# Kernel optimization log

Measured on AMD Instinct MI355X. Metric: run time of the kernel, lower is better.

Reference implementation:

```python
import jax, jax.numpy as jnp
import numpy as np
from jax import lax

B, T, E = 256, 128, 768      # batch, seq_len, bert emb dim
HE = 256                     # encoder lstm hidden (per direction)
H = 512                      # decoder hidden = 2*HE
SLOT, INTENT = 120, 64
EMB = SLOT // 3              # 40
V = SLOT + 1                 # 121, bos id = SLOT
DIN = EMB + 2 * H            # 1064 decoder lstm input
NEG = -1e12


def lstm_cell(x, h, c, Wih, Whh, bih, bhh):
    # torch gate order: i, f, g, o
    g = x @ Wih.T + h @ Whh.T + (bih + bhh)
    i, f, gg, o = jnp.split(g, 4, axis=-1)
    c = jax.nn.sigmoid(f) * c + jax.nn.sigmoid(i) * jnp.tanh(gg)
    h = jax.nn.sigmoid(o) * jnp.tanh(c)
    return h, c


def setup_inputs() -> dict:
    key = jax.random.key(0)
    ks = jax.random.split(key, 24)
    s = 0.05
    n = lambda k, shp: jax.random.normal(k, shp, jnp.float32) * s
    return {
        'seq_reps': jax.random.normal(ks[0], (B, T, E), jnp.float32),
        'nwp_index': jax.random.randint(ks[1], (B, T, 1), 0, 2),
        'slot_output_mask': jax.random.randint(ks[2], (B, T), 0, 2).astype(bool),
        'emb_table': jax.random.uniform(ks[3], (V, EMB), jnp.float32, -0.1, 0.1),
        # encoder fwd / bwd LSTM
        'Wf_ih': n(ks[4], (4 * HE, E)), 'Wf_hh': n(ks[5], (4 * HE, HE)),
        'bf_ih': n(ks[6], (4 * HE,)), 'bf_hh': n(ks[7], (4 * HE,)),
        'Wb_ih': n(ks[8], (4 * HE, E)), 'Wb_hh': n(ks[9], (4 * HE, HE)),
        'bb_ih': n(ks[10], (4 * HE,)), 'bb_hh': n(ks[11], (4 * HE,)),
        # decoder LSTM
        'Wd_ih': n(ks[12], (4 * H, DIN)), 'Wd_hh': n(ks[13], (4 * H, H)),
        'bd_ih': n(ks[14], (4 * H,)), 'bd_hh': n(ks[15], (4 * H,)),
        # attention + output heads
        'attn_W': n(ks[16], (H, H)), 'attn_b': n(ks[17], (H,)),
        'slot_W': n(ks[18], (SLOT, 2 * H)), 'slot_b': n(ks[19], (SLOT,)),
        'intent_W': n(ks[20], (INTENT, 2 * H)), 'intent_b': n(ks[21], (INTENT,)),
    }


def forward(seq_reps, nwp_index, slot_output_mask, emb_table,
            Wf_ih, Wf_hh, bf_ih, bf_hh, Wb_ih, Wb_hh, bb_ih, bb_hh,
            Wd_ih, Wd_hh, bd_ih, bd_hh, attn_W, attn_b,
            slot_W, slot_b, intent_W, intent_b):
    # ---------- Encoder: 1-layer bidirectional LSTM ----------
    xs = seq_reps.transpose(1, 0, 2)  # [T,B,E]
    z = jnp.zeros((B, HE), seq_reps.dtype)

    def fstep(carry, x):
        h, c = lstm_cell(x, carry[0], carry[1], Wf_ih, Wf_hh, bf_ih, bf_hh)
        return (h, c), h

    def bstep(carry, x):
        h, c = lstm_cell(x, carry[0], carry[1], Wb_ih, Wb_hh, bb_ih, bb_hh)
        return (h, c), h

    _, hf = lax.scan(fstep, (z, z), xs)
    _, hb = lax.scan(bstep, (z, z), xs[::-1])
    enc = jnp.concatenate([hf, hb[::-1]], -1).transpose(1, 0, 2)  # [B,T,512]

    # last real hidden: out[b, #nonzero(nwp_index[b])]
    count = jnp.clip((nwp_index[:, :, 0] != 0).sum(1), 0, T - 1)
    last_hidden = enc[jnp.arange(B), count]  # [B,H]

    # ---------- Attention (energies independent of step -> precompute) ----------
    energies = enc @ attn_W.T + attn_b  # [B,T,H]

    def attention(h):  # h: [B,H]
        e = jnp.einsum('bth,bh->bt', energies, h)
        e = jnp.where(slot_output_mask, NEG, e)
        alpha = jax.nn.softmax(e, -1)
        return jnp.einsum('bt,bth->bh', alpha, enc)  # [B,H]

    # ---------- Decoder: per-timestep LSTM + attention ----------
    bos_emb = jnp.broadcast_to(emb_table[SLOT], (B, EMB))
    zH = jnp.zeros((B, H), seq_reps.dtype)
    aligns = enc.transpose(1, 0, 2)  # [T,B,H]

    def dstep(carry, aligned):
        emb, ctx, h, c = carry
        inp = jnp.concatenate([emb, ctx, aligned], -1)  # [B,1064]
        h, c = lstm_cell(inp, h, c, Wd_ih, Wd_hh, bd_ih, bd_hh)
        score = jnp.concatenate([h, ctx], -1) @ slot_W.T + slot_b
        logp = jax.nn.log_softmax(score, -1)
        nxt = jnp.argmax(logp, -1)
        emb = emb_table[nxt]
        ctx_new = attention(h)
        return (emb, ctx_new, h, c), (logp, h, ctx_new)

    _, (logps, h_seq, ctx_seq) = lax.scan(dstep, (bos_emb, last_hidden, zH, zH), aligns)

    slot_scores = logps.transpose(1, 0, 2)  # [B,T,SLOT]
    # intent computed at step 0: intent_context == attention(h after step 0) == ctx_seq[0]
    intent_score = jnp.concatenate([h_seq[0], ctx_seq[0]], -1) @ intent_W.T + intent_b
    return slot_scores, intent_score


def reference(seq_reps, nwp_index, slot_output_mask, emb_table,
              Wf_ih, Wf_hh, bf_ih, bf_hh, Wb_ih, Wb_hh, bb_ih, bb_hh,
              Wd_ih, Wd_hh, bd_ih, bd_hh, attn_W, attn_b,
              slot_W, slot_b, intent_W, intent_b):
    return forward(seq_reps, nwp_index, slot_output_mask, emb_table,
                   Wf_ih, Wf_hh, bf_ih, bf_hh, Wb_ih, Wb_hh, bb_ih, bb_hh,
                   Wd_ih, Wd_hh, bd_ih, bd_hh, attn_W, attn_b,
                   slot_W, slot_b, intent_W, intent_b)
```

## Files before the change

kernel.cpp:

```cpp
#include <hip/hip_runtime.h>
#include <math.h>

#define Bn 256
#define Tn 128
#define En 768
#define HEn 256
#define Hn 512
#define SLOTn 120
#define INTENTn 64
#define EMBn 40
#define NEGV -1e12f

__device__ __forceinline__ float sigm(float x) { return 1.0f / (1.0f + expf(-x)); }

__global__ void zero_k(float* __restrict__ p, int n) {
    int i = blockIdx.x * blockDim.x + threadIdx.x;
    int stride = gridDim.x * blockDim.x;
    for (; i < n; i += stride) p[i] = 0.f;
}

__global__ void detect_mask_k(const unsigned char* __restrict__ m, int* __restrict__ flag) {
    __shared__ int any;
    if (threadIdx.x == 0) any = 0;
    __syncthreads();
    int found = 0;
    for (int i = threadIdx.x; i < 32768; i += 256) {
        if ((i & 3) != 0 && m[i] != 0) found = 1;
    }
    if (found) atomicOr(&any, 1);
    __syncthreads();
    if (threadIdx.x == 0) *flag = any;
}

__global__ __launch_bounds__(256) void slotwt_k(const float* __restrict__ W,
                                               float* __restrict__ wT4) {
    int idx = blockIdx.x * 256 + threadIdx.x;
    int k = idx >> 7, s = idx & 127;
    float v = (s < SLOTn) ? W[(size_t)s * 1024 + k] : 0.f;
    wT4[((size_t)(k >> 2) * 128 + s) * 4 + (k & 3)] = v;
}

__device__ __forceinline__ float4 f4zero() { float4 z; z.x = z.y = z.z = z.w = 0.f; return z; }

__device__ __forceinline__ float4 enc_wload(const float* __restrict__ Wih,
                                            const float* __restrict__ Whh,
                                            int jrow, int k) {
    return (k < En) ? *(const float4*)(Wih + (size_t)jrow * En + k)
                    : *(const float4*)(Whh + (size_t)jrow * HEn + (k - En));
}

__global__ __launch_bounds__(512) void enc_step_k(
    const float* __restrict__ seq,
    const float* __restrict__ Wf_ih, const float* __restrict__ Wf_hh,
    const float* __restrict__ bf_ih, const float* __restrict__ bf_hh,
    const float* __restrict__ Wb_ih, const float* __restrict__ Wb_hh,
    const float* __restrict__ bb_ih, const float* __restrict__ bb_hh,
    const float* __restrict__ hf_in, float* __restrict__ hf_out, float* __restrict__ cf,
    const float* __restrict__ hb_in, float* __restrict__ hb_out, float* __restrict__ cb,
    float* __restrict__ enc, int step)
{
    const int dir = blockIdx.z;
    const float* __restrict__ Wih = dir ? Wb_ih : Wf_ih;
    const float* __restrict__ Whh = dir ? Wb_hh : Wf_hh;
    const float* __restrict__ bih = dir ? bb_ih : bf_ih;
    const float* __restrict__ bhh = dir ? bb_hh : bf_hh;
    const float* __restrict__ h_in = dir ? hb_in : hf_in;
    float* __restrict__ h_out = dir ? hb_out : hf_out;
    float* __restrict__ c_st  = dir ? cb : cf;
    const int t_eff = dir ? (Tn - 1 - step) : step;

    const int jb = blockIdx.x;
    const int b0 = blockIdx.y << 5;
    const int tid = threadIdx.x;
    const int c   = tid & 63;
    const int wid = __builtin_amdgcn_readfirstlane(tid >> 6);
    const int bw  = b0 + (wid << 2);

    __shared__ float Bs[2][64][68];
    __shared__ float Gs[32][68];

    const int cs0 = tid >> 4,          kq0 = tid & 15;
    const int cs1 = (tid + 512) >> 4;
    const int j0row = ((cs0 >> 4) << 8) + (jb << 4) + (cs0 & 15);
    const int j1row = ((cs1 >> 4) << 8) + (jb << 4) + (cs1 & 15);

    float acc[4] = {0,0,0,0};

    float4 p0 = enc_wload(Wih, Whh, j0row, kq0 << 2);
    float4 p1 = enc_wload(Wih, Whh, j1row, kq0 << 2);
    *(float4*)&Bs[0][cs0][kq0 << 2] = p0;
    *(float4*)&Bs[0][cs1][kq0 << 2] = p1;
    __syncthreads();

    for (int t = 0; t < 16; ++t) {
        const int k0 = t << 6;
        const int buf = t & 1;
        if (t < 15) {
            p0 = enc_wload(Wih, Whh, j0row, k0 + 64 + (kq0 << 2));
            p1 = enc_wload(Wih, Whh, j1row, k0 + 64 + (kq0 << 2));
        }
#pragma unroll
        for (int g = 0; g < 16; ++g) {
            const int kk = k0 + (g << 2);
            const float* __restrict__ abase;
            size_t astr;
            if (kk < En) { abase = seq + ((size_t)bw * Tn + t_eff) * En + kk; astr = (size_t)Tn * En; }
            else         { abase = h_in + ((size_t)bw << 8) + (kk - En);      astr = HEn; }
            float4 bf = *(const float4*)&Bs[buf][c][g << 2];
#pragma unroll
            for (int i = 0; i < 4; ++i) {
                float4 a = *(const float4*)(abase + (size_t)i * astr);
                acc[i] += a.x * bf.x + a.y * bf.y + a.z * bf.z + a.w * bf.w;
            }
        }
        if (t < 15) {
            *(float4*)&Bs[buf ^ 1][cs0][kq0 << 2] = p0;
            *(float4*)&Bs[buf ^ 1][cs1][kq0 << 2] = p1;
        }
        __syncthreads();
    }

#pragma unroll
    for (int i = 0; i < 4; ++i) Gs[(wid << 2) + i][c] = acc[i];
    __syncthreads();

    {
        int row = tid >> 4, jl = tid & 15;
        int jg = (jb << 4) + jl;
        int b = b0 + row;
        float gi = Gs[row][jl]      + bih[jg]           + bhh[jg];
        float gf = Gs[row][16 + jl] + bih[HEn + jg]     + bhh[HEn + jg];
        float gg = Gs[row][32 + jl] + bih[2 * HEn + jg] + bhh[2 * HEn + jg];
        float go = Gs[row][48 + jl] + bih[3 * HEn + jg] + bhh[3 * HEn + jg];
        float ii = sigm(gi), ff = sigm(gf), tg = tanhf(gg), oo = sigm(go);
        int ci = (b << 8) + jg;
        float cn = ff * c_st[ci] + ii * tg;
        float hn = oo * tanhf(cn);
        c_st[ci] = cn;
        h_out[ci] = hn;
        enc[((size_t)t_eff * Bn + b) * Hn + dir * HEn + jg] = hn;
    }
}

__global__ __launch_bounds__(256) void energT_k(
    const float* __restrict__ enc, const float* __restrict__ attn_W,
    float* __restrict__ energT)
{
    const int nb = blockIdx.x;
    const int mb = blockIdx.y;
    const int t = mb >> 2, b0 = (mb & 3) << 6;
    const int tid = threadIdx.x;
    const int tx = tid & 15, ty = tid >> 4;
    __shared__ float As[32][68];
    __shared__ float Bs[32][68];
    float acc[4][4] = {};
    for (int kt = 0; kt < 16; ++kt) {
        int k0 = kt << 5;
#pragma unroll
        for (int r = 0; r < 8; ++r) {
            int idx = tid + (r << 8);
            int kk = idx & 31, row = idx >> 5;
            As[kk][row] = enc[((size_t)t * Bn + b0 + row) * Hn + k0 + kk];
            Bs[kk][row] = attn_W[(nb * 64 + row) * Hn + k0 + kk];
        }
        __syncthreads();
#pragma unroll
        for (int kk = 0; kk < 32; ++kk) {
            float a0 = As[kk][ty * 4], a1 = As[kk][ty * 4 + 1];
            float a2 = As[kk][ty * 4 + 2], a3 = As[kk][ty * 4 + 3];
            float w0 = Bs[kk][tx * 4], w1 = Bs[kk][tx * 4 + 1];
            float w2 = Bs[kk][tx * 4 + 2], w3 = Bs[kk][tx * 4 + 3];
            acc[0][0] += a0 * w0; acc[0][1] += a0 * w1; acc[0][2] += a0 * w2; acc[0][3] += a0 * w3;
            acc[1][0] += a1 * w0; acc[1][1] += a1 * w1; acc[1][2] += a1 * w2; acc[1][3] += a1 * w3;
            acc[2][0] += a2 * w0; acc[2][1] += a2 * w1; acc[2][2] += a2 * w2; acc[2][3] += a2 * w3;
            acc[3][0] += a3 * w0; acc[3][1] += a3 * w1; acc[3][2] += a3 * w2; acc[3][3] += a3 * w3;
        }
        __syncthreads();
    }
#pragma unroll
    for (int i = 0; i < 4; ++i)
#pragma unroll
        for (int q = 0; q < 4; ++q)
            energT[((size_t)(b0 + ty * 4 + i) * Hn + nb * 64 + tx * 4 + q) * Tn + t] = acc[i][q];
}

__global__ __launch_bounds__(64) void init2_k(
    const int* __restrict__ nwp, const float* __restrict__ enc,
    const float* __restrict__ emb_table,
    float* __restrict__ ctx0, float* __restrict__ embb)
{
    int b = blockIdx.x;
    int lane = threadIdx.x;
    int p1 = (nwp[b * Tn + lane] != 0);
    int p2 = (nwp[b * Tn + lane + 64] != 0);
    unsigned long long m1 = __ballot(p1), m2 = __ballot(p2);
    int cnt = __popcll(m1) + __popcll(m2);
    int idx = cnt < (Tn - 1) ? cnt : (Tn - 1);
#pragma unroll
    for (int r = 0; r < 8; ++r) {
        int j = lane + (r << 6);
        ctx0[(b << 9) + j] = enc[((size_t)idx * Bn + b) * Hn + j];
    }
    if (lane < EMBn) embb[b * EMBn + lane] = emb_table[SLOTn * EMBn + lane];
}

__device__ __forceinline__ float4 dec_wload(const float* __restrict__ Wih,
                                            const float* __restrict__ Whh,
                                            int jrow, int k) {
    if (k < 1064) return *(const float4*)(Wih + (size_t)jrow * 1064 + k);
    if (k < 1576) return *(const float4*)(Whh + ((size_t)jrow << 9) + (k - 1064));
    return f4zero();
}

__global__ __launch_bounds__(512) void dec_step_k(
    const float* __restrict__ embb, const float* __restrict__ ctx_in,
    const float* __restrict__ enc, const float* __restrict__ h_in,
    float* __restrict__ h_out, float* __restrict__ c_st,
    const float* __restrict__ Wih, const float* __restrict__ Whh,
    const float* __restrict__ bih, const float* __restrict__ bhh,
    float* __restrict__ h0_out, int step)
{
    const int jb = blockIdx.x;
    const int b0 = blockIdx.y << 5;
    const int tid = threadIdx.x;
    const int c   = tid & 63;
    const int wid = __builtin_amdgcn_readfirstlane(tid >> 6);
    const int bw  = b0 + (wid << 2);

    __shared__ float Bs[2][64][68];
    __shared__ float Gs[32][68];

    const int cs0 = tid >> 4,          kq0 = tid & 15;
    const int cs1 = (tid + 512) >> 4;
    const int j0row = ((cs0 >> 4) << 9) + (jb << 4) + (cs0 & 15);
    const int j1row = ((cs1 >> 4) << 9) + (jb << 4) + (cs1 & 15);

    float acc[4] = {0,0,0,0};

    float4 p0 = dec_wload(Wih, Whh, j0row, kq0 << 2);
    float4 p1 = dec_wload(Wih, Whh, j1row, kq0 << 2);
    *(float4*)&Bs[0][cs0][kq0 << 2] = p0;
    *(float4*)&Bs[0][cs1][kq0 << 2] = p1;
    __syncthreads();

    for (int t = 0; t < 25; ++t) {
        const int k0 = t << 6;
        const int buf = t & 1;
        if (t < 24) {
            p0 = dec_wload(Wih, Whh, j0row, k0 + 64 + (kq0 << 2));
            p1 = dec_wload(Wih, Whh, j1row, k0 + 64 + (kq0 << 2));
        }
#pragma unroll
        for (int g = 0; g < 16; ++g) {
            const int kk = k0 + (g << 2);
            if (kk < 1576) {
                const float* __restrict__ abase;
                size_t astr;
                if (kk < 40)        { abase = embb   + (size_t)bw * EMBn + kk;               astr = EMBn; }
                else if (kk < 552)  { abase = ctx_in + ((size_t)bw << 9) + (kk - 40);        astr = Hn; }
                else if (kk < 1064) { abase = enc + ((size_t)step * Bn + bw) * Hn + (kk - 552); astr = Hn; }
                else                { abase = h_in  + ((size_t)bw << 9) + (kk - 1064);       astr = Hn; }
                float4 bf = *(const float4*)&Bs[buf][c][g << 2];
#pragma unroll
                for (int i = 0; i < 4; ++i) {
                    float4 a = *(const float4*)(abase + (size_t)i * astr);
                    acc[i] += a.x * bf.x + a.y * bf.y + a.z * bf.z + a.w * bf.w;
                }
            }
        }
        if (t < 24) {
            *(float4*)&Bs[buf ^ 1][cs0][kq0 << 2] = p0;
            *(float4*)&Bs[buf ^ 1][cs1][kq0 << 2] = p1;
        }
        __syncthreads();
    }

#pragma unroll
    for (int i = 0; i < 4; ++i) Gs[(wid << 2) + i][c] = acc[i];
    __syncthreads();

    {
        int row = tid >> 4, jl = tid & 15;
        int jg = (jb << 4) + jl;
        int b = b0 + row;
        float gi = Gs[row][jl]      + bih[jg]          + bhh[jg];
        float gf = Gs[row][16 + jl] + bih[Hn + jg]     + bhh[Hn + jg];
        float gg = Gs[row][32 + jl] + bih[2 * Hn + jg] + bhh[2 * Hn + jg];
        float go = Gs[row][48 + jl] + bih[3 * Hn + jg] + bhh[3 * Hn + jg];
        float ii = sigm(gi), ff = sigm(gf), tg = tanhf(gg), oo = sigm(go);
        int ci = (b << 9) + jg;
        float cn = ff * c_st[ci] + ii * tg;
        float hn = oo * tanhf(cn);
        c_st[ci] = cn;
        h_out[ci] = hn;
        if (h0_out) h0_out[ci] = hn;
    }
}

__global__ __launch_bounds__(256) void dec_attn_slot_k(
    const float* __restrict__ enc, const float* __restrict__ energT,
    const float* __restrict__ h, const float* __restrict__ ctx_in,
    float* __restrict__ ctx_out, const unsigned char* __restrict__ mask_u8,
    const int* __restrict__ mask_i32, const int* __restrict__ mask_flag,
    const float* __restrict__ wT4, const float* __restrict__ slot_b,
    const float* __restrict__ emb_table, float* __restrict__ embb,
    float* __restrict__ out_slot, float* __restrict__ ctx0_save, int step)
{
    __shared__ float hs[512];
    __shared__ float red2[8][132];
    __shared__ float es[128];
    __shared__ float redm[2];
    __shared__ float ctxp[2][512];
    __shared__ float pacc[2][8][132];
    __shared__ float sc[8][132];
    __shared__ float logZ[8];
    __shared__ int amax[8];

    const int bid = blockIdx.x;
    const int tid = threadIdx.x;

    if (bid < Bn) {
        const int b = bid;
        hs[tid] = h[(b << 9) + tid];
        hs[tid + 256] = h[(b << 9) + 256 + tid];
        __syncthreads();
        {
            const int tg = tid & 31, jg = tid >> 5;
            const float* __restrict__ ep = energT + ((size_t)b * Hn + jg * 64) * Tn + (tg << 2);
            float4 a = f4zero();
#pragma unroll 8
            for (int jj = 0; jj < 64; ++jj) {
                float hv = hs[jg * 64 + jj];
                float4 e4 = *(const float4*)(ep + (size_t)jj * Tn);
                a.x += e4.x * hv; a.y += e4.y * hv; a.z += e4.z * hv; a.w += e4.w * hv;
            }
            *(float4*)&red2[jg][tg << 2] = a;
        }
        __syncthreads();
        if (tid < 128) {
            float e = 0.f;
#pragma unroll
            for (int jg = 0; jg < 8; ++jg) e += red2[jg][tid];
            bool mv = (*mask_flag) ? (mask_u8[(size_t)b * Tn + tid] != 0)
                                   : (mask_i32[(size_t)b * Tn + tid] != 0);
            es[tid] = mv ? NEGV : e;
        }
        __syncthreads();
        if (tid < 64) {
            float v = fmaxf(es[tid], es[tid + 64]);
            for (int o = 32; o; o >>= 1) v = fmaxf(v, __shfl_down(v, o));
            if (tid == 0) redm[0] = v;
        }
        __syncthreads();
        float m = redm[0];
        if (tid < 128) es[tid] = __expf(es[tid] - m);
        __syncthreads();
        if (tid < 64) {
            float v = es[tid] + es[tid + 64];
            for (int o = 32; o; o >>= 1) v += __shfl_down(v, o);
            if (tid == 0) redm[0] = v;
        }
        __syncthreads();
        float inv = 1.0f / redm[0];
        if (tid < 128) es[tid] *= inv;
        __syncthreads();
        {
            const int dq = tid & 127, th = tid >> 7;
            const int d = dq << 2;
            const float* __restrict__ ep2 = enc + (b << 9) + d;
            float4 a = f4zero();
            const int tbase = th << 6;
#pragma unroll 8
            for (int t2 = 0; t2 < 64; ++t2) {
                float al = es[tbase + t2];
                float4 e4 = *(const float4*)(ep2 + (size_t)(tbase + t2) * (Bn * Hn));
                a.x += al * e4.x; a.y += al * e4.y; a.z += al * e4.z; a.w += al * e4.w;
            }
            *(float4*)&ctxp[th][d] = a;
        }
        __syncthreads();
        {
            float v0 = ctxp[0][tid] + ctxp[1][tid];
            float v1 = ctxp[0][tid + 256] + ctxp[1][tid + 256];
            ctx_out[(b << 9) + tid] = v0;
            ctx_out[(b << 9) + 256 + tid] = v1;
            if (ctx0_save) {
                ctx0_save[(b << 9) + tid] = v0;
                ctx0_save[(b << 9) + 256 + tid] = v1;
            }
        }
    } else {
        const int b_base = (bid - Bn) << 3;
        const int sl = tid & 127;
        const int kg = __builtin_amdgcn_readfirstlane(tid >> 7);
        const float* __restrict__ a0 = (kg ? ctx_in : h) + ((size_t)b_base << 9);
        const float* __restrict__ wb = wT4 + (size_t)kg * 128 * 128 * 4;
        float acc[8] = {0,0,0,0,0,0,0,0};
        for (int k4 = 0; k4 < 128; ++k4) {
            const int k = k4 << 2;
            float4 w4 = *(const float4*)(wb + ((size_t)k4 * 128 + sl) * 4);
#pragma unroll
            for (int i = 0; i < 8; ++i) {
                const float* __restrict__ ar = a0 + ((size_t)i << 9) + k;
                acc[i] += w4.x * ar[0] + w4.y * ar[1] + w4.z * ar[2] + w4.w * ar[3];
            }
        }
#pragma unroll
        for (int i = 0; i < 8; ++i) pacc[kg][i][sl] = acc[i];
        __syncthreads();
        if (tid < 128) {
            float sb = (tid < SLOTn) ? slot_b[tid] : 0.f;
#pragma unroll
            for (int i = 0; i < 8; ++i)
                sc[i][tid] = pacc[0][i][tid] + pacc[1][i][tid] + sb;
        }
        __syncthreads();
        if (tid < 8) {
            float mm = -INFINITY; int am = 0;
            for (int ss = 0; ss < SLOTn; ++ss) {
                float v = sc[tid][ss];
                if (v > mm) { mm = v; am = ss; }
            }
            float sum = 0.f;
            for (int ss = 0; ss < SLOTn; ++ss) sum += __expf(sc[tid][ss] - mm);
            logZ[tid] = mm + logf(sum);
            amax[tid] = am;
        }
        __syncthreads();
        for (int r = 0; r < 4; ++r) {
            int idx = tid + (r << 8);
            int bl = idx >> 7, ss = idx & 127;
            if (ss < SLOTn)
                out_slot[(size_t)(b_base + bl) * Tn * SLOTn + step * SLOTn + ss] =
                    sc[bl][ss] - logZ[bl];
        }
        for (int i = tid; i < 8 * EMBn; i += 256) {
            int bl = i / EMBn, e2 = i % EMBn;
            embb[(b_base + bl) * EMBn + e2] = emb_table[amax[bl] * EMBn + e2];
        }
    }
}

__global__ __launch_bounds__(256) void intent_k(
    const float* __restrict__ h0, const float* __restrict__ ctx0,
    const float* __restrict__ W, const float* __restrict__ bias,
    float* __restrict__ out)
{
    __shared__ float ins[8][1032];
    __shared__ float Ws[16][68];
    const int tid = threadIdx.x;
    const int b_base = blockIdx.x << 3;
    for (int r = 0; r < 32; ++r) {
        int idx = tid + (r << 8);
        int bl = idx >> 10, k = idx & 1023;
        int b = b_base + bl;
        ins[bl][k] = (k < 512) ? h0[(b << 9) + k] : ctx0[(b << 9) + (k - 512)];
    }
    __syncthreads();
    const int n = tid & 63, bq = tid >> 6;
    float acc0 = 0.f, acc1 = 0.f;
    for (int kt = 0; kt < 64; ++kt) {
        int k0 = kt << 4;
#pragma unroll
        for (int r = 0; r < 4; ++r) {
            int idx = tid + (r << 8);
            int kk = idx & 15, nn = idx >> 4;
            Ws[kk][nn] = W[nn * 1024 + k0 + kk];
        }
        __syncthreads();
#pragma unroll
        for (int kk = 0; kk < 16; ++kk) {
            float w = Ws[kk][n];
            acc0 += w * ins[bq * 2][k0 + kk];
            acc1 += w * ins[bq * 2 + 1][k0 + kk];
        }
        __syncthreads();
    }
    out[(b_base + bq * 2) * INTENTn + n] = acc0 + bias[n];
    out[(b_base + bq * 2 + 1) * INTENTn + n] = acc1 + bias[n];
}

extern "C" void kernel_launch(void* const* d_in, const int* in_sizes, int n_in,
                              void* d_out, int out_size, void* d_ws, size_t ws_size,
                              hipStream_t stream) {
    (void)in_sizes; (void)n_in; (void)out_size; (void)ws_size;

    const float* seq      = (const float*)d_in[0];
    const int*   nwp      = (const int*)d_in[1];
    const unsigned char* mask_u8 = (const unsigned char*)d_in[2];
    const int*   mask_i32 = (const int*)d_in[2];
    const float* embt     = (const float*)d_in[3];
    const float* Wf_ih    = (const float*)d_in[4];
    const float* Wf_hh    = (const float*)d_in[5];
    const float* bf_ih    = (const float*)d_in[6];
    const float* bf_hh    = (const float*)d_in[7];
    const float* Wb_ih    = (const float*)d_in[8];
    const float* Wb_hh    = (const float*)d_in[9];
    const float* bb_ih    = (const float*)d_in[10];
    const float* bb_hh    = (const float*)d_in[11];
    const float* Wd_ih    = (const float*)d_in[12];
    const float* Wd_hh    = (const float*)d_in[13];
    const float* bd_ih    = (const float*)d_in[14];
    const float* bd_hh    = (const float*)d_in[15];
    const float* attn_W   = (const float*)d_in[16];
    const float* slot_W   = (const float*)d_in[18];
    const float* slot_b   = (const float*)d_in[19];
    const float* intent_W = (const float*)d_in[20];
    const float* intent_b = (const float*)d_in[21];

    float* Wp = (float*)d_ws;
    size_t off = 0;
    float* enc    = Wp + off; off += (size_t)Tn * Bn * Hn;
    float* energT = Wp + off; off += (size_t)Bn * Hn * Tn;
    float* zbase  = Wp + off;
    float* hf0 = Wp + off; off += Bn * HEn;
    float* hf1 = Wp + off; off += Bn * HEn;
    float* cf  = Wp + off; off += Bn * HEn;
    float* hb0 = Wp + off; off += Bn * HEn;
    float* hb1 = Wp + off; off += Bn * HEn;
    float* cb  = Wp + off; off += Bn * HEn;
    float* hd0 = Wp + off; off += Bn * Hn;
    float* hd1 = Wp + off; off += Bn * Hn;
    float* cd  = Wp + off; off += Bn * Hn;
    int nzero = (int)(Wp + off - zbase);
    float* ctx0b = Wp + off; off += Bn * Hn;
    float* ctx1b = Wp + off; off += Bn * Hn;
    float* h0s   = Wp + off; off += Bn * Hn;
    float* ctx0s = Wp + off; off += Bn * Hn;
    float* embb  = Wp + off; off += Bn * EMBn;
    int* mask_flag = (int*)(Wp + off); off += 1;
    float* wT4   = Wp + off; off += 1024 * 128;

    float* out = (float*)d_out;

    zero_k<<<512, 256, 0, stream>>>(zbase, nzero);
    detect_mask_k<<<1, 256, 0, stream>>>(mask_u8, mask_flag);
    slotwt_k<<<512, 256, 0, stream>>>(slot_W, wT4);

    for (int s = 0; s < Tn; ++s) {
        const float* hinf = (s & 1) ? hf1 : hf0;
        float* houtf      = (s & 1) ? hf0 : hf1;
        const float* hinb = (s & 1) ? hb1 : hb0;
        float* houtb      = (s & 1) ? hb0 : hb1;
        enc_step_k<<<dim3(16, 8, 2), 512, 0, stream>>>(
            seq, Wf_ih, Wf_hh, bf_ih, bf_hh, Wb_ih, Wb_hh, bb_ih, bb_hh,
            hinf, houtf, cf, hinb, houtb, cb, enc, s);
    }

    energT_k<<<dim3(8, 512), 256, 0, stream>>>(enc, attn_W, energT);
    init2_k<<<256, 64, 0, stream>>>(nwp, enc, embt, ctx0b, embb);

    for (int t = 0; t < Tn; ++t) {
        const float* ctxin = (t & 1) ? ctx1b : ctx0b;
        float* ctxout      = (t & 1) ? ctx0b : ctx1b;
        const float* hin   = (t & 1) ? hd1 : hd0;
        float* hout        = (t & 1) ? hd0 : hd1;
        dec_step_k<<<dim3(32, 8), 512, 0, stream>>>(
            embb, ctxin, enc, hin, hout, cd,
            Wd_ih, Wd_hh, bd_ih, bd_hh, (t == 0) ? h0s : (float*)nullptr, t);
        dec_attn_slot_k<<<288, 256, 0, stream>>>(
            enc, energT, hout, ctxin, ctxout, mask_u8, mask_i32, mask_flag,
            wT4, slot_b, embt, embb, out, (t == 0) ? ctx0s : (float*)nullptr, t);
    }

    intent_k<<<32, 256, 0, stream>>>(h0s, ctx0s, intent_W, intent_b,
                                     out + (size_t)Bn * Tn * SLOTn);
}
```

Before: 48.63 ms.

## Fuse all stages into one persistent kernel with software grid barriers

Replaces the roughly 260 per-timestep kernel launches (encoder steps, energy GEMM, decoder step plus attention/slot) with a single persistent kernel of 256 blocks. Stages are separated by an atomic-counter grid barrier. The aim is to remove launch overhead and inter-kernel gaps on a recurrence that is dominated by launch latency. The risks are deadlock if all 256 blocks cannot be co-resident, the cost of each spin barrier, and a fixed work partition that may leave some compute units idle.

```diff
diff --git a/kernel.cpp b/kernel.cpp
--- a/kernel.cpp
+++ b/kernel.cpp
@@ -10,198 +10,47 @@
 #define INTENTn 64
 #define EMBn 40
 #define NEGV -1e12f
+#define NBLK 256
+#define NTHR 512
 
 __device__ __forceinline__ float sigm(float x) { return 1.0f / (1.0f + expf(-x)); }
 
-__global__ void zero_k(float* __restrict__ p, int n) {
-    int i = blockIdx.x * blockDim.x + threadIdx.x;
-    int stride = gridDim.x * blockDim.x;
-    for (; i < n; i += stride) p[i] = 0.f;
+__device__ __forceinline__ float4 f4zero() { float4 z; z.x = z.y = z.z = z.w = 0.f; return z; }
+
+__global__ void prezero_k(unsigned* __restrict__ p) {
+    if (threadIdx.x < 8) p[threadIdx.x] = 0u;
 }
 
-__global__ void detect_mask_k(const unsigned char* __restrict__ m, int* __restrict__ flag) {
-    __shared__ int any;
-    if (threadIdx.x == 0) any = 0;
+__device__ __forceinline__ void gsync(unsigned* bar, unsigned* gen) {
     __syncthreads();
-    int found = 0;
-    for (int i = threadIdx.x; i < 32768; i += 256) {
-        if ((i & 3) != 0 && m[i] != 0) found = 1;
-    }
-    if (found) atomicOr(&any, 1);
+    if (threadIdx.x == 0) {
+        __threadfence();
+        unsigned g = __hip_atomic_load(gen, __ATOMIC_RELAXED, __HIP_MEMORY_SCOPE_AGENT);
+        unsigned a = __hip_atomic_fetch_add(bar, 1u, __ATOMIC_ACQ_REL, __HIP_MEMORY_SCOPE_AGENT) + 1u;
+        if (a == (unsigned)NBLK) {
+            __hip_atomic_store(bar, 0u, __ATOMIC_RELAXED, __HIP_MEMORY_SCOPE_AGENT);
+            __hip_atomic_store(gen, g + 1u, __ATOMIC_RELEASE, __HIP_MEMORY_SCOPE_AGENT);
+        } else {
+            while (__hip_atomic_load(gen, __ATOMIC_ACQUIRE, __HIP_MEMORY_SCOPE_AGENT) == g)
+                __builtin_amdgcn_s_sleep(8);
+        }
+        __threadfence();
+    }
     __syncthreads();
-    if (threadIdx.x == 0) *flag = any;
 }
 
-__global__ __launch_bounds__(256) void slotwt_k(const float* __restrict__ W,
-                                               float* __restrict__ wT4) {
-    int idx = blockIdx.x * 256 + threadIdx.x;
-    int k = idx >> 7, s = idx & 127;
-    float v = (s < SLOTn) ? W[(size_t)s * 1024 + k] : 0.f;
-    wT4[((size_t)(k >> 2) * 128 + s) * 4 + (k & 3)] = v;
-}
-
-__device__ __forceinline__ float4 f4zero() { float4 z; z.x = z.y = z.z = z.w = 0.f; return z; }
+struct SmemGemm { float Bs[2][64][68]; float Gs[32][68]; };
+struct SmemEn   { float As[2][32][68]; float Bs2[2][32][68]; };
+struct SmemAttn { float hs[512]; float red2[8][132]; float es[128];
+                  float pacc2[2][128]; float sc[128]; float ctxp[4][512];
+                  float logZ; int amax; };
+struct SmemInt  { float pacc[8][64]; };
 
 __device__ __forceinline__ float4 enc_wload(const float* __restrict__ Wih,
                                             const float* __restrict__ Whh,
                                             int jrow, int k) {
     return (k < En) ? *(const float4*)(Wih + (size_t)jrow * En + k)
                     : *(const float4*)(Whh + (size_t)jrow * HEn + (k - En));
-}
-
-__global__ __launch_bounds__(512) void enc_step_k(
-    const float* __restrict__ seq,
-    const float* __restrict__ Wf_ih, const float* __restrict__ Wf_hh,
-    const float* __restrict__ bf_ih, const float* __restrict__ bf_hh,
-    const float* __restrict__ Wb_ih, const float* __restrict__ Wb_hh,
-    const float* __restrict__ bb_ih, const float* __restrict__ bb_hh,
-    const float* __restrict__ hf_in, float* __restrict__ hf_out, float* __restrict__ cf,
-    const float* __restrict__ hb_in, float* __restrict__ hb_out, float* __restrict__ cb,
-    float* __restrict__ enc, int step)
-{
-    const int dir = blockIdx.z;
-    const float* __restrict__ Wih = dir ? Wb_ih : Wf_ih;
-    const float* __restrict__ Whh = dir ? Wb_hh : Wf_hh;
-    const float* __restrict__ bih = dir ? bb_ih : bf_ih;
-    const float* __restrict__ bhh = dir ? bb_hh : bf_hh;
-    const float* __restrict__ h_in = dir ? hb_in : hf_in;
-    float* __restrict__ h_out = dir ? hb_out : hf_out;
-    float* __restrict__ c_st  = dir ? cb : cf;
-    const int t_eff = dir ? (Tn - 1 - step) : step;
-
-    const int jb = blockIdx.x;
-    const int b0 = blockIdx.y << 5;
-    const int tid = threadIdx.x;
-    const int c   = tid & 63;
-    const int wid = __builtin_amdgcn_readfirstlane(tid >> 6);
-    const int bw  = b0 + (wid << 2);
-
-    __shared__ float Bs[2][64][68];
-    __shared__ float Gs[32][68];
-
-    const int cs0 = tid >> 4,          kq0 = tid & 15;
-    const int cs1 = (tid + 512) >> 4;
-    const int j0row = ((cs0 >> 4) << 8) + (jb << 4) + (cs0 & 15);
-    const int j1row = ((cs1 >> 4) << 8) + (jb << 4) + (cs1 & 15);
-
-    float acc[4] = {0,0,0,0};
-
-    float4 p0 = enc_wload(Wih, Whh, j0row, kq0 << 2);
-    float4 p1 = enc_wload(Wih, Whh, j1row, kq0 << 2);
-    *(float4*)&Bs[0][cs0][kq0 << 2] = p0;
-    *(float4*)&Bs[0][cs1][kq0 << 2] = p1;
-    __syncthreads();
-
-    for (int t = 0; t < 16; ++t) {
-        const int k0 = t << 6;
-        const int buf = t & 1;
-        if (t < 15) {
-            p0 = enc_wload(Wih, Whh, j0row, k0 + 64 + (kq0 << 2));
-            p1 = enc_wload(Wih, Whh, j1row, k0 + 64 + (kq0 << 2));
-        }
-#pragma unroll
-        for (int g = 0; g < 16; ++g) {
-            const int kk = k0 + (g << 2);
-            const float* __restrict__ abase;
-            size_t astr;
-            if (kk < En) { abase = seq + ((size_t)bw * Tn + t_eff) * En + kk; astr = (size_t)Tn * En; }
-            else         { abase = h_in + ((size_t)bw << 8) + (kk - En);      astr = HEn; }
-            float4 bf = *(const float4*)&Bs[buf][c][g << 2];
-#pragma unroll
-            for (int i = 0; i < 4; ++i) {
-                float4 a = *(const float4*)(abase + (size_t)i * astr);
-                acc[i] += a.x * bf.x + a.y * bf.y + a.z * bf.z + a.w * bf.w;
-            }
-        }
-        if (t < 15) {
-            *(float4*)&Bs[buf ^ 1][cs0][kq0 << 2] = p0;
-            *(float4*)&Bs[buf ^ 1][cs1][kq0 << 2] = p1;
-        }
-        __syncthreads();
-    }
-
-#pragma unroll
-    for (int i = 0; i < 4; ++i) Gs[(wid << 2) + i][c] = acc[i];
-    __syncthreads();
-
-    {
-        int row = tid >> 4, jl = tid & 15;
-        int jg = (jb << 4) + jl;
-        int b = b0 + row;
-        float gi = Gs[row][jl]      + bih[jg]           + bhh[jg];
-        float gf = Gs[row][16 + jl] + bih[HEn + jg]     + bhh[HEn + jg];
-        float gg = Gs[row][32 + jl] + bih[2 * HEn + jg] + bhh[2 * HEn + jg];
-        float go = Gs[row][48 + jl] + bih[3 * HEn + jg] + bhh[3 * HEn + jg];
-        float ii = sigm(gi), ff = sigm(gf), tg = tanhf(gg), oo = sigm(go);
-        int ci = (b << 8) + jg;
-        float cn = ff * c_st[ci] + ii * tg;
-        float hn = oo * tanhf(cn);
-        c_st[ci] = cn;
-        h_out[ci] = hn;
-        enc[((size_t)t_eff * Bn + b) * Hn + dir * HEn + jg] = hn;
-    }
-}
-
-__global__ __launch_bounds__(256) void energT_k(
-    const float* __restrict__ enc, const float* __restrict__ attn_W,
-    float* __restrict__ energT)
-{
-    const int nb = blockIdx.x;
-    const int mb = blockIdx.y;
-    const int t = mb >> 2, b0 = (mb & 3) << 6;
-    const int tid = threadIdx.x;
-    const int tx = tid & 15, ty = tid >> 4;
-    __shared__ float As[32][68];
-    __shared__ float Bs[32][68];
-    float acc[4][4] = {};
-    for (int kt = 0; kt < 16; ++kt) {
-        int k0 = kt << 5;
-#pragma unroll
-        for (int r = 0; r < 8; ++r) {
-            int idx = tid + (r << 8);
-            int kk = idx & 31, row = idx >> 5;
-            As[kk][row] = enc[((size_t)t * Bn + b0 + row) * Hn + k0 + kk];
-            Bs[kk][row] = attn_W[(nb * 64 + row) * Hn + k0 + kk];
-        }
-        __syncthreads();
-#pragma unroll
-        for (int kk = 0; kk < 32; ++kk) {
-            float a0 = As[kk][ty * 4], a1 = As[kk][ty * 4 + 1];
-            float a2 = As[kk][ty * 4 + 2], a3 = As[kk][ty * 4 + 3];
-            float w0 = Bs[kk][tx * 4], w1 = Bs[kk][tx * 4 + 1];
-            float w2 = Bs[kk][tx * 4 + 2], w3 = Bs[kk][tx * 4 + 3];
-            acc[0][0] += a0 * w0; acc[0][1] += a0 * w1; acc[0][2] += a0 * w2; acc[0][3] += a0 * w3;
-            acc[1][0] += a1 * w0; acc[1][1] += a1 * w1; acc[1][2] += a1 * w2; acc[1][3] += a1 * w3;
-            acc[2][0] += a2 * w0; acc[2][1] += a2 * w1; acc[2][2] += a2 * w2; acc[2][3] += a2 * w3;
-            acc[3][0] += a3 * w0; acc[3][1] += a3 * w1; acc[3][2] += a3 * w2; acc[3][3] += a3 * w3;
-        }
-        __syncthreads();
-    }
-#pragma unroll
-    for (int i = 0; i < 4; ++i)
-#pragma unroll
-        for (int q = 0; q < 4; ++q)
-            energT[((size_t)(b0 + ty * 4 + i) * Hn + nb * 64 + tx * 4 + q) * Tn + t] = acc[i][q];
-}
-
-__global__ __launch_bounds__(64) void init2_k(
-    const int* __restrict__ nwp, const float* __restrict__ enc,
-    const float* __restrict__ emb_table,
-    float* __restrict__ ctx0, float* __restrict__ embb)
-{
-    int b = blockIdx.x;
-    int lane = threadIdx.x;
-    int p1 = (nwp[b * Tn + lane] != 0);
-    int p2 = (nwp[b * Tn + lane + 64] != 0);
-    unsigned long long m1 = __ballot(p1), m2 = __ballot(p2);
-    int cnt = __popcll(m1) + __popcll(m2);
-    int idx = cnt < (Tn - 1) ? cnt : (Tn - 1);
-#pragma unroll
-    for (int r = 0; r < 8; ++r) {
-        int j = lane + (r << 6);
-        ctx0[(b << 9) + j] = enc[((size_t)idx * Bn + b) * Hn + j];
-    }
-    if (lane < EMBn) embb[b * EMBn + lane] = emb_table[SLOTn * EMBn + lane];
 }
 
 __device__ __forceinline__ float4 dec_wload(const float* __restrict__ Wih,
@@ -212,272 +61,385 @@
     return f4zero();
 }
 
-__global__ __launch_bounds__(512) void dec_step_k(
-    const float* __restrict__ embb, const float* __restrict__ ctx_in,
-    const float* __restrict__ enc, const float* __restrict__ h_in,
-    float* __restrict__ h_out, float* __restrict__ c_st,
-    const float* __restrict__ Wih, const float* __restrict__ Whh,
-    const float* __restrict__ bih, const float* __restrict__ bhh,
-    float* __restrict__ h0_out, int step)
+extern "C" __global__ __launch_bounds__(NTHR, 4) void mega_k(
+    const float* __restrict__ seq, const int* __restrict__ nwp,
+    const unsigned char* __restrict__ mask_u8, const int* __restrict__ mask_i32,
+    const float* __restrict__ embt,
+    const float* __restrict__ Wf_ih, const float* __restrict__ Wf_hh,
+    const float* __restrict__ bf_ih, const float* __restrict__ bf_hh,
+    const float* __restrict__ Wb_ih, const float* __restrict__ Wb_hh,
+    const float* __restrict__ bb_ih, const float* __restrict__ bb_hh,
+    const float* __restrict__ Wd_ih, const float* __restrict__ Wd_hh,
+    const float* __restrict__ bd_ih, const float* __restrict__ bd_hh,
+    const float* __restrict__ attn_W, const float* __restrict__ slot_W,
+    const float* __restrict__ slot_b,
+    const float* __restrict__ intent_W, const float* __restrict__ intent_b,
+    float* __restrict__ enc, float* __restrict__ energT,
+    float* hf0, float* hf1, float* cf, float* hb0, float* hb1, float* cb,
+    float* hd0, float* hd1, float* cd,
+    float* ctx0b, float* ctx1b, float* h0s, float* ctx0s, float* embb,
+    float* wT4, float* zbase, int nzero,
+    unsigned* bar, unsigned* gen, int* mflag,
+    float* out_slot, float* out_intent)
 {
-    const int jb = blockIdx.x;
-    const int b0 = blockIdx.y << 5;
-    const int tid = threadIdx.x;
-    const int c   = tid & 63;
-    const int wid = __builtin_amdgcn_readfirstlane(tid >> 6);
-    const int bw  = b0 + (wid << 2);
-
-    __shared__ float Bs[2][64][68];
-    __shared__ float Gs[32][68];
-
-    const int cs0 = tid >> 4,          kq0 = tid & 15;
-    const int cs1 = (tid + 512) >> 4;
-    const int j0row = ((cs0 >> 4) << 9) + (jb << 4) + (cs0 & 15);
-    const int j1row = ((cs1 >> 4) << 9) + (jb << 4) + (cs1 & 15);
-
-    float acc[4] = {0,0,0,0};
-
-    float4 p0 = dec_wload(Wih, Whh, j0row, kq0 << 2);
-    float4 p1 = dec_wload(Wih, Whh, j1row, kq0 << 2);
-    *(float4*)&Bs[0][cs0][kq0 << 2] = p0;
-    *(float4*)&Bs[0][cs1][kq0 << 2] = p1;
-    __syncthreads();
-
-    for (int t = 0; t < 25; ++t) {
-        const int k0 = t << 6;
-        const int buf = t & 1;
-        if (t < 24) {
-            p0 = dec_wload(Wih, Whh, j0row, k0 + 64 + (kq0 << 2));
-            p1 = dec_wload(Wih, Whh, j1row, k0 + 64 + (kq0 << 2));
-        }
-#pragma unroll
-        for (int g = 0; g < 16; ++g) {
-            const int kk = k0 + (g << 2);
-            if (kk < 1576) {
-                const float* __restrict__ abase;
-                size_t astr;
-                if (kk < 40)        { abase = embb   + (size_t)bw * EMBn + kk;               astr = EMBn; }
-                else if (kk < 552)  { abase = ctx_in + ((size_t)bw << 9) + (kk - 40);        astr = Hn; }
-                else if (kk < 1064) { abase = enc + ((size_t)step * Bn + bw) * Hn + (kk - 552); astr = Hn; }
-                else                { abase = h_in  + ((size_t)bw << 9) + (kk - 1064);       astr = Hn; }
-                float4 bf = *(const float4*)&Bs[buf][c][g << 2];
-#pragma unroll
-                for (int i = 0; i < 4; ++i) {
-                    float4 a = *(const float4*)(abase + (size_t)i * astr);
-                    acc[i] += a.x * bf.x + a.y * bf.y + a.z * bf.z + a.w * bf.w;
-                }
-            }
-        }
-        if (t < 24) {
-            *(float4*)&Bs[buf ^ 1][cs0][kq0 << 2] = p0;
-            *(float4*)&Bs[buf ^ 1][cs1][kq0 << 2] = p1;
-        }
-        __syncthreads();
-    }
-
-#pragma unroll
-    for (int i = 0; i < 4; ++i) Gs[(wid << 2) + i][c] = acc[i];
-    __syncthreads();
-
-    {
-        int row = tid >> 4, jl = tid & 15;
-        int jg = (jb << 4) + jl;
-        int b = b0 + row;
-        float gi = Gs[row][jl]      + bih[jg]          + bhh[jg];
-        float gf = Gs[row][16 + jl] + bih[Hn + jg]     + bhh[Hn + jg];
-        float gg = Gs[row][32 + jl] + bih[2 * Hn + jg] + bhh[2 * Hn + jg];
-        float go = Gs[row][48 + jl] + bih[3 * Hn + jg] + bhh[3 * Hn + jg];
-        float ii = sigm(gi), ff = sigm(gf), tg = tanhf(gg), oo = sigm(go);
-        int ci = (b << 9) + jg;
-        float cn = ff * c_st[ci] + ii * tg;
-        float hn = oo * tanhf(cn);
-        c_st[ci] = cn;
-        h_out[ci] = hn;
-        if (h0_out) h0_out[ci] = hn;
-    }
-}
-
-__global__ __launch_bounds__(256) void dec_attn_slot_k(
-    const float* __restrict__ enc, const float* __restrict__ energT,
-    const float* __restrict__ h, const float* __restrict__ ctx_in,
-    float* __restrict__ ctx_out, const unsigned char* __restrict__ mask_u8,
-    const int* __restrict__ mask_i32, const int* __restrict__ mask_flag,
-    const float* __restrict__ wT4, const float* __restrict__ slot_b,
-    const float* __restrict__ emb_table, float* __restrict__ embb,
-    float* __restrict__ out_slot, float* __restrict__ ctx0_save, int step)
-{
-    __shared__ float hs[512];
-    __shared__ float red2[8][132];
-    __shared__ float es[128];
-    __shared__ float redm[2];
-    __shared__ float ctxp[2][512];
-    __shared__ float pacc[2][8][132];
-    __shared__ float sc[8][132];
-    __shared__ float logZ[8];
-    __shared__ int amax[8];
-
+    __shared__ __align__(16) char smraw[sizeof(SmemGemm)];
     const int bid = blockIdx.x;
     const int tid = threadIdx.x;
 
-    if (bid < Bn) {
-        const int b = bid;
-        hs[tid] = h[(b << 9) + tid];
-        hs[tid + 256] = h[(b << 9) + 256 + tid];
-        __syncthreads();
-        {
-            const int tg = tid & 31, jg = tid >> 5;
-            const float* __restrict__ ep = energT + ((size_t)b * Hn + jg * 64) * Tn + (tg << 2);
-            float4 a = f4zero();
-#pragma unroll 8
-            for (int jj = 0; jj < 64; ++jj) {
-                float hv = hs[jg * 64 + jj];
-                float4 e4 = *(const float4*)(ep + (size_t)jj * Tn);
-                a.x += e4.x * hv; a.y += e4.y * hv; a.z += e4.z * hv; a.w += e4.w * hv;
-            }
-            *(float4*)&red2[jg][tg << 2] = a;
-        }
-        __syncthreads();
-        if (tid < 128) {
-            float e = 0.f;
-#pragma unroll
-            for (int jg = 0; jg < 8; ++jg) e += red2[jg][tid];
-            bool mv = (*mask_flag) ? (mask_u8[(size_t)b * Tn + tid] != 0)
-                                   : (mask_i32[(size_t)b * Tn + tid] != 0);
-            es[tid] = mv ? NEGV : e;
+    for (int i = bid * NTHR + tid; i < nzero; i += NBLK * NTHR) zbase[i] = 0.f;
+    {
+        int idx = bid * NTHR + tid;
+        int k = idx >> 7, s = idx & 127;
+        float v = (s < SLOTn) ? slot_W[(size_t)s * 1024 + k] : 0.f;
+        wT4[((size_t)(k >> 2) * 128 + s) * 4 + (k & 3)] = v;
+    }
+    if (bid == 0) {
+        int found = 0;
+        for (int i = tid; i < 32768; i += NTHR)
+            if ((i & 3) != 0 && mask_u8[i] != 0) found = 1;
+        if (found) atomicOr(mflag, 1);
+    }
+    gsync(bar, gen);
+
+    {
+        const int dir = bid >> 7;
+        const int jb  = bid & 15;
+        const int b0  = ((bid >> 4) & 7) << 5;
+        const float* __restrict__ Wih = dir ? Wb_ih : Wf_ih;
+        const float* __restrict__ Whh = dir ? Wb_hh : Wf_hh;
+        const float* __restrict__ bih = dir ? bb_ih : bf_ih;
+        const float* __restrict__ bhh = dir ? bb_hh : bf_hh;
+        float* __restrict__ c_st = dir ? cb : cf;
+        SmemGemm* sg = (SmemGemm*)smraw;
+
+        const int c   = tid & 63;
+        const int wid = tid >> 6;
+        const int bw  = b0 + (wid << 2);
+        const int cs0 = tid >> 4, kq0 = tid & 15;
+        const int cs1 = cs0 + 32;
+        const int j0row = ((cs0 >> 4) << 8) + (jb << 4) + (cs0 & 15);
+        const int j1row = ((cs1 >> 4) << 8) + (jb << 4) + (cs1 & 15);
+
+        for (int s = 0; s < Tn; ++s) {
+            const float* __restrict__ h_in = (s & 1) ? (dir ? hb1 : hf1) : (dir ? hb0 : hf0);
+            float* __restrict__ h_out      = (s & 1) ? (dir ? hb0 : hf0) : (dir ? hb1 : hf1);
+            const int t_eff = dir ? (Tn - 1 - s) : s;
+
+            float acc[4] = {0, 0, 0, 0};
+            float4 p0 = enc_wload(Wih, Whh, j0row, kq0 << 2);
+            float4 p1 = enc_wload(Wih, Whh, j1row, kq0 << 2);
+            *(float4*)&sg->Bs[0][cs0][kq0 << 2] = p0;
+            *(float4*)&sg->Bs[0][cs1][kq0 << 2] = p1;
+            __syncthreads();
+
+            for (int kt = 0; kt < 16; ++kt) {
+                const int k0 = kt << 6;
+                const int buf = kt & 1;
+                if (kt < 15) {
+                    p0 = enc_wload(Wih, Whh, j0row, k0 + 64 + (kq0 << 2));
+                    p1 = enc_wload(Wih, Whh, j1row, k0 + 64 + (kq0 << 2));
+                }
+#pragma unroll
+                for (int g = 0; g < 16; ++g) {
+                    const int kk = k0 + (g << 2);
+                    const float* __restrict__ abase;
+                    size_t astr;
+                    if (kk < En) { abase = seq + ((size_t)bw * Tn + t_eff) * En + kk; astr = (size_t)Tn * En; }
+                    else         { abase = h_in + ((size_t)bw << 8) + (kk - En);      astr = HEn; }
+                    float4 bf = *(const float4*)&sg->Bs[buf][c][g << 2];
+#pragma unroll
+                    for (int i = 0; i < 4; ++i) {
+                        float4 a = *(const float4*)(abase + (size_t)i * astr);
+                        acc[i] += a.x * bf.x + a.y * bf.y + a.z * bf.z + a.w * bf.w;
+                    }
+                }
+                if (kt < 15) {
+                    *(float4*)&sg->Bs[buf ^ 1][cs0][kq0 << 2] = p0;
+                    *(float4*)&sg->Bs[buf ^ 1][cs1][kq0 << 2] = p1;
+                }
+                __syncthreads();
+            }
+
+#pragma unroll
+            for (int i = 0; i < 4; ++i) sg->Gs[(wid << 2) + i][c] = acc[i];
+            __syncthreads();
+            {
+                int row = tid >> 4, jl = tid & 15;
+                int jg = (jb << 4) + jl;
+                int b = b0 + row;
+                float gi = sg->Gs[row][jl]      + bih[jg]           + bhh[jg];
+                float gf = sg->Gs[row][16 + jl] + bih[HEn + jg]     + bhh[HEn + jg];
+                float gg = sg->Gs[row][32 + jl] + bih[2 * HEn + jg] + bhh[2 * HEn + jg];
+                float go = sg->Gs[row][48 + jl] + bih[3 * HEn + jg] + bhh[3 * HEn + jg];
+                float ii = sigm(gi), ff = sigm(gf), tg = tanhf(gg), oo = sigm(go);
+                int ci = (b << 8) + jg;
+                float cn = ff * c_st[ci] + ii * tg;
+                float hn = oo * tanhf(cn);
+                c_st[ci] = cn;
+                h_out[ci] = hn;
+                enc[((size_t)t_eff * Bn + b) * Hn + dir * HEn + jg] = hn;
+            }
+            gsync(bar, gen);
+        }
+    }
+
+    {
+        SmemEn* se = (SmemEn*)smraw;
+        const int half = tid >> 8;
+        const int htid = tid & 255;
+        const int tx = htid & 15, ty = htid >> 4;
+        const int hslot = (bid << 1) | half;
+        float (*As)[68]  = se->As[half];
+        float (*Bsp)[68] = se->Bs2[half];
+
+        for (int it = 0; it < 8; ++it) {
+            const int job = hslot + (it << 9);
+            const int nb = job & 7, mb = job >> 3;
+            const int t = mb >> 2, b0j = (mb & 3) << 6;
+            float acc[4][4] = {};
+            for (int kt = 0; kt < 16; ++kt) {
+                int k0 = kt << 5;
+#pragma unroll
+                for (int r = 0; r < 8; ++r) {
+                    int idx = htid + (r << 8);
+                    int kk = idx & 31, row = idx >> 5;
+                    As[kk][row]  = enc[((size_t)t * Bn + b0j + row) * Hn + k0 + kk];
+                    Bsp[kk][row] = attn_W[(nb * 64 + row) * Hn + k0 + kk];
+                }
+                __syncthreads();
+#pragma unroll
+                for (int kk = 0; kk < 32; ++kk) {
+                    float a0 = As[kk][ty * 4], a1 = As[kk][ty * 4 + 1];
+                    float a2 = As[kk][ty * 4 + 2], a3 = As[kk][ty * 4 + 3];
+                    float w0 = Bsp[kk][tx * 4], w1 = Bsp[kk][tx * 4 + 1];
+                    float w2 = Bsp[kk][tx * 4 + 2], w3 = Bsp[kk][tx * 4 + 3];
+                    acc[0][0] += a0 * w0; acc[0][1] += a0 * w1; acc[0][2] += a0 * w2; acc[0][3] += a0 * w3;
+                    acc[1][0] += a1 * w0; acc[1][1] += a1 * w1; acc[1][2] += a1 * w2; acc[1][3] += a1 * w3;
+                    acc[2][0] += a2 * w0; acc[2][1] += a2 * w1; acc[2][2] += a2 * w2; acc[2][3] += a2 * w3;
+                    acc[3][0] += a3 * w0; acc[3][1] += a3 * w1; acc[3][2] += a3 * w2; acc[3][3] += a3 * w3;
+                }
+                __syncthreads();
+            }
+#pragma unroll
+            for (int i = 0; i < 4; ++i)
+#pragma unroll
+                for (int q = 0; q < 4; ++q)
+                    energT[((size_t)(b0j + ty * 4 + i) * Hn + nb * 64 + tx * 4 + q) * Tn + t] = acc[i][q];
         }
         __syncthreads();
         if (tid < 64) {
-            float v = fmaxf(es[tid], es[tid + 64]);
-            for (int o = 32; o; o >>= 1) v = fmaxf(v, __shfl_down(v, o));
-            if (tid == 0) redm[0] = v;
-        }
-        __syncthreads();
-        float m = redm[0];
-        if (tid < 128) es[tid] = __expf(es[tid] - m);
+            int b = bid, lane = tid;
+            int p1 = (nwp[b * Tn + lane] != 0);
+            int p2 = (nwp[b * Tn + lane + 64] != 0);
+            unsigned long long m1 = __ballot(p1), m2 = __ballot(p2);
+            int cnt = __popcll(m1) + __popcll(m2);
+            int idx = cnt < (Tn - 1) ? cnt : (Tn - 1);
+#pragma unroll
+            for (int r = 0; r < 8; ++r) {
+                int j = lane + (r << 6);
+                ctx0b[(b << 9) + j] = enc[((size_t)idx * Bn + b) * Hn + j];
+            }
+            if (lane < EMBn) embb[b * EMBn + lane] = embt[SLOTn * EMBn + lane];
+        }
+    }
+    gsync(bar, gen);
+
+    for (int t = 0; t < Tn; ++t) {
+        const float* __restrict__ ctxin = (t & 1) ? ctx1b : ctx0b;
+        float* __restrict__ ctxout      = (t & 1) ? ctx0b : ctx1b;
+        const float* __restrict__ hin   = (t & 1) ? hd1 : hd0;
+        float* __restrict__ hout        = (t & 1) ? hd0 : hd1;
+
+        {
+            SmemGemm* sg = (SmemGemm*)smraw;
+            const int jb = bid & 31;
+            const int b0 = (bid >> 5) << 5;
+            const int c   = tid & 63;
+            const int wid = tid >> 6;
+            const int bw  = b0 + (wid << 2);
+            const int cs0 = tid >> 4, kq0 = tid & 15;
+            const int cs1 = cs0 + 32;
+            const int j0row = ((cs0 >> 4) << 9) + (jb << 4) + (cs0 & 15);
+            const int j1row = ((cs1 >> 4) << 9) + (jb << 4) + (cs1 & 15);
+
+            float acc[4] = {0, 0, 0, 0};
+            float4 p0 = dec_wload(Wd_ih, Wd_hh, j0row, kq0 << 2);
+            float4 p1 = dec_wload(Wd_ih, Wd_hh, j1row, kq0 << 2);
+            *(float4*)&sg->Bs[0][cs0][kq0 << 2] = p0;
+            *(float4*)&sg->Bs[0][cs1][kq0 << 2] = p1;
+            __syncthreads();
+
+            for (int kt = 0; kt < 25; ++kt) {
+                const int k0 = kt << 6;
+                const int buf = kt & 1;
+                if (kt < 24) {
+                    p0 = dec_wload(Wd_ih, Wd_hh, j0row, k0 + 64 + (kq0 << 2));
+                    p1 = dec_wload(Wd_ih, Wd_hh, j1row, k0 + 64 + (kq0 << 2));
+                }
+#pragma unroll
+                for (int g = 0; g < 16; ++g) {
+                    const int kk = k0 + (g << 2);
+                    if (kk < 1576) {
+                        const float* __restrict__ abase;
+                        size_t astr;
+                        if (kk < 40)        { abase = embb  + (size_t)bw * EMBn + kk;                  astr = EMBn; }
+                        else if (kk < 552)  { abase = ctxin + ((size_t)bw << 9) + (kk - 40);           astr = Hn; }
+                        else if (kk < 1064) { abase = enc + ((size_t)t * Bn + bw) * Hn + (kk - 552);   astr = Hn; }
+                        else                { abase = hin   + ((size_t)bw << 9) + (kk - 1064);         astr = Hn; }
+                        float4 bf = *(const float4*)&sg->Bs[buf][c][g << 2];
+#pragma unroll
+                        for (int i = 0; i < 4; ++i) {
+                            float4 a = *(const float4*)(abase + (size_t)i * astr);
+                            acc[i] += a.x * bf.x + a.y * bf.y + a.z * bf.z + a.w * bf.w;
+                        }
+                    }
+                }
+                if (kt < 24) {
+                    *(float4*)&sg->Bs[buf ^ 1][cs0][kq0 << 2] = p0;
+                    *(float4*)&sg->Bs[buf ^ 1][cs1][kq0 << 2] = p1;
+                }
+                __syncthreads();
+            }
+
+#pragma unroll
+            for (int i = 0; i < 4; ++i) sg->Gs[(wid << 2) + i][c] = acc[i];
+            __syncthreads();
+            {
+                int row = tid >> 4, jl = tid & 15;
+                int jg = ((bid & 31) << 4) + jl;
+                int b = ((bid >> 5) << 5) + row;
+                float gi = sg->Gs[row][jl]      + bd_ih[jg]          + bd_hh[jg];
+                float gf = sg->Gs[row][16 + jl] + bd_ih[Hn + jg]     + bd_hh[Hn + jg];
+                float gg = sg->Gs[row][32 + jl] + bd_ih[2 * Hn + jg] + bd_hh[2 * Hn + jg];
+                float go = sg->Gs[row][48 + jl] + bd_ih[3 * Hn + jg] + bd_hh[3 * Hn + jg];
+                float ii = sigm(gi), ff = sigm(gf), tg = tanhf(gg), oo = sigm(go);
+                int ci = (b << 9) + jg;
+                float cn = ff * cd[ci] + ii * tg;
+                float hn = oo * tanhf(cn);
+                cd[ci] = cn;
+                hout[ci] = hn;
+                if (t == 0) h0s[ci] = hn;
+            }
+        }
+        gsync(bar, gen);
+
+        {
+            SmemAttn* sa = (SmemAttn*)smraw;
+            const int b = bid;
+            sa->hs[tid] = hout[(b << 9) + tid];
+            __syncthreads();
+            if (tid < 256) {
+                const int tg = tid & 31, jg = tid >> 5;
+                const float* __restrict__ ep = energT + ((size_t)b * Hn + jg * 64) * Tn + (tg << 2);
+                float4 a = f4zero();
+#pragma unroll 8
+                for (int jj = 0; jj < 64; ++jj) {
+                    float hv = sa->hs[jg * 64 + jj];
+                    float4 e4 = *(const float4*)(ep + (size_t)jj * Tn);
+                    a.x += e4.x * hv; a.y += e4.y * hv; a.z += e4.z * hv; a.w += e4.w * hv;
+                }
+                *(float4*)&sa->red2[jg][tg << 2] = a;
+            } else {
+                const int sl = tid & 127;
+                const int kg = (tid >> 7) & 1;
+                const float* __restrict__ a0 = (kg ? ctxin : hout) + ((size_t)b << 9);
+                const float* __restrict__ wb = wT4 + (size_t)kg * 128 * 128 * 4;
+                float acc = 0.f;
+                for (int k4 = 0; k4 < 128; ++k4) {
+                    float4 w4 = *(const float4*)(wb + ((size_t)k4 * 128 + sl) * 4);
+                    const float* __restrict__ ar = a0 + (k4 << 2);
+                    acc += w4.x * ar[0] + w4.y * ar[1] + w4.z * ar[2] + w4.w * ar[3];
+                }
+                sa->pacc2[kg][sl] = acc;
+            }
+            __syncthreads();
+            if (tid < 128) {
+                float e = 0.f;
+#pragma unroll
+                for (int jg = 0; jg < 8; ++jg) e += sa->red2[jg][tid];
+                bool mv = (*mflag) ? (mask_u8[(size_t)b * Tn + tid] != 0)
+                                   : (mask_i32[(size_t)b * Tn + tid] != 0);
+                sa->es[tid] = mv ? NEGV : e;
+            } else if (tid >= 256 && tid < 384) {
+                int sl = tid - 256;
+                sa->sc[sl] = sa->pacc2[0][sl] + sa->pacc2[1][sl] + (sl < SLOTn ? slot_b[sl] : 0.f);
+            }
+            __syncthreads();
+            if (tid < 64) {
+                float v0 = sa->es[tid], v1 = sa->es[tid + 64];
+                float m = fmaxf(v0, v1);
+                for (int o = 32; o; o >>= 1) m = fmaxf(m, __shfl_xor(m, o));
+                float q0 = __expf(v0 - m), q1 = __expf(v1 - m);
+                float s = q0 + q1;
+                for (int o = 32; o; o >>= 1) s += __shfl_xor(s, o);
+                float inv = 1.f / s;
+                sa->es[tid] = q0 * inv; sa->es[tid + 64] = q1 * inv;
+            } else if (tid == 256) {
+                float mm = -INFINITY; int am = 0;
+                for (int ss = 0; ss < SLOTn; ++ss) { float v = sa->sc[ss]; if (v > mm) { mm = v; am = ss; } }
+                float sum = 0.f;
+                for (int ss = 0; ss < SLOTn; ++ss) sum += __expf(sa->sc[ss] - mm);
+                sa->logZ = mm + logf(sum);
+                sa->amax = am;
+            }
+            __syncthreads();
+            {
+                const int th = tid >> 7;
+                const int d = (tid & 127) << 2;
+                const float* __restrict__ ep2 = enc + (b << 9) + d;
+                const int tb = th << 5;
+                float4 a = f4zero();
+#pragma unroll 8
+                for (int t2 = 0; t2 < 32; ++t2) {
+                    float al = sa->es[tb + t2];
+                    float4 e4 = *(const float4*)(ep2 + (size_t)(tb + t2) * (Bn * Hn));
+                    a.x += al * e4.x; a.y += al * e4.y; a.z += al * e4.z; a.w += al * e4.w;
+                }
+                *(float4*)&sa->ctxp[th][d] = a;
+            }
+            __syncthreads();
+            if (tid < 128) {
+                int d = tid << 2;
+                float4 s0 = *(float4*)&sa->ctxp[0][d];
+                float4 s1 = *(float4*)&sa->ctxp[1][d];
+                float4 s2 = *(float4*)&sa->ctxp[2][d];
+                float4 s3 = *(float4*)&sa->ctxp[3][d];
+                float4 r;
+                r.x = s0.x + s1.x + s2.x + s3.x;
+                r.y = s0.y + s1.y + s2.y + s3.y;
+                r.z = s0.z + s1.z + s2.z + s3.z;
+                r.w = s0.w + s1.w + s2.w + s3.w;
+                *(float4*)(ctxout + (b << 9) + d) = r;
+                if (t == 0) *(float4*)(ctx0s + (b << 9) + d) = r;
+            } else if (tid >= 128 && tid < 128 + SLOTn) {
+                int ss = tid - 128;
+                out_slot[(size_t)b * Tn * SLOTn + t * SLOTn + ss] = sa->sc[ss] - sa->logZ;
+            } else if (tid >= 256 && tid < 256 + EMBn) {
+                int e2 = tid - 256;
+                embb[b * EMBn + e2] = embt[sa->amax * EMBn + e2];
+            }
+        }
+        gsync(bar, gen);
+    }
+
+    {
+        SmemInt* si = (SmemInt*)smraw;
+        const int n = tid & 63, kg = tid >> 6;
+        const float* __restrict__ act = (kg < 4) ? (h0s + (bid << 9) + (kg << 7))
+                                                 : (ctx0s + (bid << 9) + ((kg - 4) << 7));
+        const float* __restrict__ wr = intent_W + n * 1024 + (kg << 7);
+        float acc = 0.f;
+#pragma unroll 4
+        for (int kk = 0; kk < 128; ++kk) acc += wr[kk] * act[kk];
+        si->pacc[kg][n] = acc;
         __syncthreads();
         if (tid < 64) {
-            float v = es[tid] + es[tid + 64];
-            for (int o = 32; o; o >>= 1) v += __shfl_down(v, o);
-            if (tid == 0) redm[0] = v;
-        }
-        __syncthreads();
-        float inv = 1.0f / redm[0];
-        if (tid < 128) es[tid] *= inv;
-        __syncthreads();
-        {
-            const int dq = tid & 127, th = tid >> 7;
-            const int d = dq << 2;
-            const float* __restrict__ ep2 = enc + (b << 9) + d;
-            float4 a = f4zero();
-            const int tbase = th << 6;
-#pragma unroll 8
-            for (int t2 = 0; t2 < 64; ++t2) {
-                float al = es[tbase + t2];
-                float4 e4 = *(const float4*)(ep2 + (size_t)(tbase + t2) * (Bn * Hn));
-                a.x += al * e4.x; a.y += al * e4.y; a.z += al * e4.z; a.w += al * e4.w;
-            }
-            *(float4*)&ctxp[th][d] = a;
-        }
-        __syncthreads();
-        {
-            float v0 = ctxp[0][tid] + ctxp[1][tid];
-            float v1 = ctxp[0][tid + 256] + ctxp[1][tid + 256];
-            ctx_out[(b << 9) + tid] = v0;
-            ctx_out[(b << 9) + 256 + tid] = v1;
-            if (ctx0_save) {
-                ctx0_save[(b << 9) + tid] = v0;
-                ctx0_save[(b << 9) + 256 + tid] = v1;
-            }
-        }
-    } else {
-        const int b_base = (bid - Bn) << 3;
-        const int sl = tid & 127;
-        const int kg = __builtin_amdgcn_readfirstlane(tid >> 7);
-        const float* __restrict__ a0 = (kg ? ctx_in : h) + ((size_t)b_base << 9);
-        const float* __restrict__ wb = wT4 + (size_t)kg * 128 * 128 * 4;
-        float acc[8] = {0,0,0,0,0,0,0,0};
-        for (int k4 = 0; k4 < 128; ++k4) {
-            const int k = k4 << 2;
-            float4 w4 = *(const float4*)(wb + ((size_t)k4 * 128 + sl) * 4);
-#pragma unroll
-            for (int i = 0; i < 8; ++i) {
-                const float* __restrict__ ar = a0 + ((size_t)i << 9) + k;
-                acc[i] += w4.x * ar[0] + w4.y * ar[1] + w4.z * ar[2] + w4.w * ar[3];
-            }
-        }
-#pragma unroll
-        for (int i = 0; i < 8; ++i) pacc[kg][i][sl] = acc[i];
-        __syncthreads();
-        if (tid < 128) {
-            float sb = (tid < SLOTn) ? slot_b[tid] : 0.f;
-#pragma unroll
-            for (int i = 0; i < 8; ++i)
-                sc[i][tid] = pacc[0][i][tid] + pacc[1][i][tid] + sb;
-        }
-        __syncthreads();
-        if (tid < 8) {
-            float mm = -INFINITY; int am = 0;
-            for (int ss = 0; ss < SLOTn; ++ss) {
-                float v = sc[tid][ss];
-                if (v > mm) { mm = v; am = ss; }
-            }
-            float sum = 0.f;
-            for (int ss = 0; ss < SLOTn; ++ss) sum += __expf(sc[tid][ss] - mm);
-            logZ[tid] = mm + logf(sum);
-            amax[tid] = am;
-        }
-        __syncthreads();
-        for (int r = 0; r < 4; ++r) {
-            int idx = tid + (r << 8);
-            int bl = idx >> 7, ss = idx & 127;
-            if (ss < SLOTn)
-                out_slot[(size_t)(b_base + bl) * Tn * SLOTn + step * SLOTn + ss] =
-                    sc[bl][ss] - logZ[bl];
-        }
-        for (int i = tid; i < 8 * EMBn; i += 256) {
-            int bl = i / EMBn, e2 = i % EMBn;
-            embb[(b_base + bl) * EMBn + e2] = emb_table[amax[bl] * EMBn + e2];
-        }
-    }
-}
-
-__global__ __launch_bounds__(256) void intent_k(
-    const float* __restrict__ h0, const float* __restrict__ ctx0,
-    const float* __restrict__ W, const float* __restrict__ bias,
-    float* __restrict__ out)
-{
-    __shared__ float ins[8][1032];
-    __shared__ float Ws[16][68];
-    const int tid = threadIdx.x;
-    const int b_base = blockIdx.x << 3;
-    for (int r = 0; r < 32; ++r) {
-        int idx = tid + (r << 8);
-        int bl = idx >> 10, k = idx & 1023;
-        int b = b_base + bl;
-        ins[bl][k] = (k < 512) ? h0[(b << 9) + k] : ctx0[(b << 9) + (k - 512)];
-    }
-    __syncthreads();
-    const int n = tid & 63, bq = tid >> 6;
-    float acc0 = 0.f, acc1 = 0.f;
-    for (int kt = 0; kt < 64; ++kt) {
-        int k0 = kt << 4;
-#pragma unroll
-        for (int r = 0; r < 4; ++r) {
-            int idx = tid + (r << 8);
-            int kk = idx & 15, nn = idx >> 4;
-            Ws[kk][nn] = W[nn * 1024 + k0 + kk];
-        }
-        __syncthreads();
-#pragma unroll
-        for (int kk = 0; kk < 16; ++kk) {
-            float w = Ws[kk][n];
-            acc0 += w * ins[bq * 2][k0 + kk];
-            acc1 += w * ins[bq * 2 + 1][k0 + kk];
-        }
-        __syncthreads();
-    }
-    out[(b_base + bq * 2) * INTENTn + n] = acc0 + bias[n];
-    out[(b_base + bq * 2 + 1) * INTENTn + n] = acc1 + bias[n];
+            float s = 0.f;
+#pragma unroll
+            for (int kg2 = 0; kg2 < 8; ++kg2) s += si->pacc[kg2][tid];
+            out_intent[bid * INTENTn + tid] = s + intent_b[tid];
+        }
+    }
 }
 
 extern "C" void kernel_launch(void* const* d_in, const int* in_sizes, int n_in,
@@ -528,41 +490,25 @@
     float* h0s   = Wp + off; off += Bn * Hn;
     float* ctx0s = Wp + off; off += Bn * Hn;
     float* embb  = Wp + off; off += Bn * EMBn;
-    int* mask_flag = (int*)(Wp + off); off += 1;
     float* wT4   = Wp + off; off += 1024 * 128;
+    unsigned* barp = (unsigned*)(Wp + off); off += 8;
+    unsigned* bar  = barp + 0;
+    unsigned* gen  = barp + 1;
+    int*      mflag = (int*)(barp + 2);
 
     float* out = (float*)d_out;
-
-    zero_k<<<512, 256, 0, stream>>>(zbase, nzero);
-    detect_mask_k<<<1, 256, 0, stream>>>(mask_u8, mask_flag);
-    slotwt_k<<<512, 256, 0, stream>>>(slot_W, wT4);
-
-    for (int s = 0; s < Tn; ++s) {
-        const float* hinf = (s & 1) ? hf1 : hf0;
-        float* houtf      = (s & 1) ? hf0 : hf1;
-        const float* hinb = (s & 1) ? hb1 : hb0;
-        float* houtb      = (s & 1) ? hb0 : hb1;
-        enc_step_k<<<dim3(16, 8, 2), 512, 0, stream>>>(
-            seq, Wf_ih, Wf_hh, bf_ih, bf_hh, Wb_ih, Wb_hh, bb_ih, bb_hh,
-            hinf, houtf, cf, hinb, houtb, cb, enc, s);
-    }
-
-    energT_k<<<dim3(8, 512), 256, 0, stream>>>(enc, attn_W, energT);
-    init2_k<<<256, 64, 0, stream>>>(nwp, enc, embt, ctx0b, embb);
-
-    for (int t = 0; t < Tn; ++t) {
-        const float* ctxin = (t & 1) ? ctx1b : ctx0b;
-        float* ctxout      = (t & 1) ? ctx0b : ctx1b;
-        const float* hin   = (t & 1) ? hd1 : hd0;
-        float* hout        = (t & 1) ? hd0 : hd1;
-        dec_step_k<<<dim3(32, 8), 512, 0, stream>>>(
-            embb, ctxin, enc, hin, hout, cd,
-            Wd_ih, Wd_hh, bd_ih, bd_hh, (t == 0) ? h0s : (float*)nullptr, t);
-        dec_attn_slot_k<<<288, 256, 0, stream>>>(
-            enc, energT, hout, ctxin, ctxout, mask_u8, mask_i32, mask_flag,
-            wT4, slot_b, embt, embb, out, (t == 0) ? ctx0s : (float*)nullptr, t);
-    }
-
-    intent_k<<<32, 256, 0, stream>>>(h0s, ctx0s, intent_W, intent_b,
-                                     out + (size_t)Bn * Tn * SLOTn);
+    float* out_intent = out + (size_t)Bn * Tn * SLOTn;
+
+    prezero_k<<<1, 64, 0, stream>>>(barp);
+    mega_k<<<NBLK, NTHR, 0, stream>>>(
+        seq, nwp, mask_u8, mask_i32, embt,
+        Wf_ih, Wf_hh, bf_ih, bf_hh, Wb_ih, Wb_hh, bb_ih, bb_hh,
+        Wd_ih, Wd_hh, bd_ih, bd_hh,
+        attn_W, slot_W, slot_b, intent_W, intent_b,
+        enc, energT,
+        hf0, hf1, cf, hb0, hb1, cb, hd0, hd1, cd,
+        ctx0b, ctx1b, h0s, ctx0s, embb,
+        wT4, zbase, nzero,
+        bar, gen, mflag,
+        out, out_intent);
 }
```

Result: slower. 178.3 ms (+266.6%).
